# Kernel optimization log

Hardware: AMD Instinct MI355X
Metric: run time of the kernel (lower is better)

Reference implementation:

```python
import jax, jax.numpy as jnp
import numpy as np

RX = 2  # matches init rx
RY = 2  # matches init ry


def _bilinear_gather(img, coords):
    """Bilinear sample with zero padding (mirrors grid_sample align_corners=True, padding_mode='zeros').
    img: [C,H,W]; coords: [P,2] pixel-space (x,y). Returns [C,P]."""
    C, H, W = img.shape
    x, y = coords[:, 0], coords[:, 1]
    x0, y0 = jnp.floor(x), jnp.floor(y)
    wx, wy = x - x0, y - y0

    def tap(xi, yi, w):
        valid = (xi >= 0) & (xi <= W - 1) & (yi >= 0) & (yi <= H - 1)
        xc = jnp.clip(xi, 0, W - 1).astype(jnp.int32)
        yc = jnp.clip(yi, 0, H - 1).astype(jnp.int32)
        v = img[:, yc, xc]  # [C,P] gather
        return v * (w * valid.astype(w.dtype))[None, :]

    return (tap(x0, y0, (1 - wx) * (1 - wy)) + tap(x0 + 1, y0, wx * (1 - wy))
            + tap(x0, y0 + 1, (1 - wx) * wy) + tap(x0 + 1, y0 + 1, wx * wy))


def _local_cost_volume(flow, f1, f2, rx, ry):
    """build_sample_cv: windowed bilinear gather of f2 around (grid + flow), dot with f1.
    Returns cv [N,H,W,2ry+1,2rx+1] with window ordered (dy,dx)."""
    N, C, H, W = f1.shape
    dt = f1.dtype
    gy, gx = jnp.meshgrid(jnp.arange(H, dtype=dt), jnp.arange(W, dtype=dt), indexing='ij')
    base = jnp.stack([gx, gy], 0)[None]            # [1,2,H,W] (x,y) like coords_grid
    cen = (base + flow).transpose(0, 2, 3, 1)       # [N,H,W,2]
    dx = jnp.linspace(-rx, rx, 2 * rx + 1).astype(dt)
    dy = jnp.linspace(-ry, ry, 2 * ry + 1).astype(dt)
    mgy, mgx = jnp.meshgrid(dy, dx, indexing='ij')  # [dH,dW]
    off = jnp.stack([mgx, mgy], -1)                 # [dH,dW,2] (x,y)
    dH, dW = 2 * ry + 1, 2 * rx + 1
    coords = cen[:, None, None] + off[None, :, :, None, None, :]  # [N,dH,dW,H,W,2]
    coords = coords.reshape(N, dH * dW * H * W, 2)
    samp = jax.vmap(_bilinear_gather)(f2, coords)   # [N,C,dH*dW*H*W]
    samp = samp.reshape(N, C, dH, dW, H, W)
    # cv[n,h,w,i,j] = sum_c f1[n,c,h,w] * f2_sampled[n,c,i,j,h,w]
    cv = jnp.einsum('nchw,ncijhw->nhwij', f1, samp)
    return cv


def setup_inputs() -> dict:
    key = jax.random.key(0)
    k1, k2, k3 = jax.random.split(key, 3)
    N, C, H, W = 2, 256, 55, 128
    return {
        'flow': jax.random.normal(k1, (N, 2, H, W), dtype=jnp.float32),
        'f1': jax.random.normal(k2, (N, C, H, W), dtype=jnp.float32),
        'f2': jax.random.normal(k3, (N, C, H, W), dtype=jnp.float32),
    }


def reference(flow, f1, f2):
    cv = _local_cost_volume(flow, f1, f2, RX, RY)   # [N,H,W,dH,dW]
    N, H, W, dH, dW = cv.shape
    flat = cv.reshape(N, H, W, dH * dW)
    # WTA over the last two (window) dims, as in get_argmax_NHW_xy_last_th
    wta_val = jnp.max(flat, axis=-1)
    idx = jnp.argmax(flat, axis=-1)
    wta_xy = jnp.stack([idx % dW, idx // dW], axis=0)  # [2,N,H,W] (x,y)
    return cv, wta_val, wta_xy
```

## Files before the change

kernel.cpp:

```cpp
#include <hip/hip_runtime.h>

#define N_   2
#define C_   256
#define H_   55
#define W_   128
#define HW_  (H_ * W_)
#define NPIX (N_ * HW_)

#define OFF_CV  0
#define OFF_VAL (NPIX * 25)
#define OFF_XY  (OFF_VAL + NPIX)

__global__ __launch_bounds__(256) void transpose_kernel(const float* __restrict__ f1,
                                                        const float* __restrict__ f2,
                                                        float* __restrict__ f1t,
                                                        float* __restrict__ f2t) {
    __shared__ float tile[64][65];
    const int z = blockIdx.z;
    const int n = z & 1;
    const float* __restrict__ src = (z & 2) ? f2 : f1;
    float* __restrict__ dst = (z & 2) ? f2t : f1t;
    src += (size_t)n * C_ * HW_;
    dst += (size_t)n * C_ * HW_;

    const int p0 = blockIdx.x * 64;
    const int c0 = blockIdx.y * 64;
    const int q = threadIdx.x & 15;
    const int r = threadIdx.x >> 4;

    #pragma unroll
    for (int rr = r; rr < 64; rr += 16) {
        const float4 v = *(const float4*)(src + (size_t)(c0 + rr) * HW_ + p0 + q * 4);
        tile[rr][q * 4 + 0] = v.x;
        tile[rr][q * 4 + 1] = v.y;
        tile[rr][q * 4 + 2] = v.z;
        tile[rr][q * 4 + 3] = v.w;
    }
    __syncthreads();

    #pragma unroll
    for (int j = 0; j < 4; ++j) {
        const int pr = r + 16 * j;
        float4 v;
        v.x = tile[q * 4 + 0][pr];
        v.y = tile[q * 4 + 1][pr];
        v.z = tile[q * 4 + 2][pr];
        v.w = tile[q * 4 + 3][pr];
        *(float4*)(dst + (size_t)(p0 + pr) * C_ + c0 + q * 4) = v;
    }
}

__device__ __forceinline__ float dot4(const float4 a, const float4 b) {
    return a.x * b.x + a.y * b.y + a.z * b.z + a.w * b.w;
}

__global__ __launch_bounds__(256) void costvol_kernel(const float* __restrict__ flow,
                                                      const float* __restrict__ f1t,
                                                      const float* __restrict__ f2t,
                                                      float* __restrict__ out) {
    __shared__ float Dsh[4][36];

    const int wv   = threadIdx.x >> 6;
    const int lane = threadIdx.x & 63;
    const int sgrp = lane >> 4;
    const int cgrp = lane & 15;
    const int pix  = blockIdx.x * 4 + wv;
    const int n    = pix / HW_;
    const int rem  = pix - n * HW_;
    const int h    = rem >> 7;
    const int w    = rem & (W_ - 1);

    const float4* __restrict__ arow = (const float4*)(f1t + (size_t)pix * C_) + cgrp * 4;
    const float4 a0 = arow[0], a1 = arow[1], a2 = arow[2], a3 = arow[3];

    const float fx = flow[((size_t)(n * 2 + 0) * H_ + h) * W_ + w];
    const float fy = flow[((size_t)(n * 2 + 1) * H_ + h) * W_ + w];
    const float cx = (float)w + fx;
    const float cy = (float)h + fy;
    const float x0f = floorf(cx), y0f = floorf(cy);
    const float wx = cx - x0f,   wy = cy - y0f;
    const int ix0 = (int)x0f,    iy0 = (int)y0f;

    const float4* __restrict__ f2base =
        (const float4*)(f2t + (size_t)n * HW_ * C_);

    #pragma unroll
    for (int p = 0; p < 9; ++p) {
        const int s  = p * 4 + sgrp;
        const int ly = s / 6, lx = s - ly * 6;
        const int sy = iy0 - 2 + ly;
        const int sx = ix0 - 2 + lx;
        float part = 0.f;
        if (sy >= 0 && sy < H_ && sx >= 0 && sx < W_) {
            const float4* __restrict__ b =
                f2base + (size_t)(sy * W_ + sx) * (C_ / 4) + cgrp * 4;
            part = dot4(a0, b[0]) + dot4(a1, b[1]) + dot4(a2, b[2]) + dot4(a3, b[3]);
        }
        part += __shfl_xor(part, 1, 64);
        part += __shfl_xor(part, 2, 64);
        part += __shfl_xor(part, 4, 64);
        part += __shfl_xor(part, 8, 64);
        if (cgrp == 0) Dsh[wv][s] = part;
    }
    __syncthreads();

    float cv = 0.f;
    if (lane < 25) {
        const int i = lane / 5, j = lane - i * 5;
        const float D00 = Dsh[wv][i * 6 + j];
        const float D01 = Dsh[wv][i * 6 + j + 1];
        const float D10 = Dsh[wv][i * 6 + j + 6];
        const float D11 = Dsh[wv][i * 6 + j + 7];
        cv = (1.f - wx) * (1.f - wy) * D00 + wx * (1.f - wy) * D01
           + (1.f - wx) * wy * D10 + wx * wy * D11;
        out[OFF_CV + (size_t)pix * 25 + lane] = cv;
    }

    float v  = (lane < 25) ? cv : -3.4e38f;
    int  idx = (lane < 25) ? lane : 25;
    #pragma unroll
    for (int off = 16; off >= 1; off >>= 1) {
        const float v2 = __shfl_down(v, off, 32);
        const int   i2 = __shfl_down(idx, off, 32);
        if (v2 > v || (v2 == v && i2 < idx)) { v = v2; idx = i2; }
    }
    if (lane == 0) {
        out[OFF_VAL + pix] = v;
        out[OFF_XY + pix]        = (float)(idx % 5);
        out[OFF_XY + NPIX + pix] = (float)(idx / 5);
    }
}

extern "C" void kernel_launch(void* const* d_in, const int* in_sizes, int n_in,
                              void* d_out, int out_size, void* d_ws, size_t ws_size,
                              hipStream_t stream) {
    const float* flow = (const float*)d_in[0];
    const float* f1   = (const float*)d_in[1];
    const float* f2   = (const float*)d_in[2];
    float* out = (float*)d_out;

    float* f1t = (float*)d_ws;
    float* f2t = f1t + (size_t)N_ * HW_ * C_;

    transpose_kernel<<<dim3(HW_ / 64, C_ / 64, 4), 256, 0, stream>>>(f1, f2, f1t, f2t);
    costvol_kernel<<<dim3(NPIX / 4), 256, 0, stream>>>(flow, f1t, f2t, out);
}
```

Measured before the change: 115.6 us.

## Drop f1 transpose and stage f1 via shared memory; remap blocks per XCD

The separate transpose of f1 is removed. Each cost-volume block now loads its 4 pixels' 256 channels straight from NCHW f1 with one float4 per thread into shared memory, which halves the transpose kernel's traffic. Blocks are also remapped so that consecutive pixel ranges go to the same XCD, aiming to improve L2 locality for the f2t window gathers. The cost is a block-wide sync, and the f1 reads are strided by HW, with each thread reading a 16-byte chunk from a different channel row.

```diff
diff --git a/kernel.cpp b/kernel.cpp
--- a/kernel.cpp
+++ b/kernel.cpp
@@ -6,22 +6,19 @@
 #define W_   128
 #define HW_  (H_ * W_)
 #define NPIX (N_ * HW_)
+#define NBLK (NPIX / 4)
+#define BPX  (NBLK / 8)
 
 #define OFF_CV  0
 #define OFF_VAL (NPIX * 25)
 #define OFF_XY  (OFF_VAL + NPIX)
 
-__global__ __launch_bounds__(256) void transpose_kernel(const float* __restrict__ f1,
-                                                        const float* __restrict__ f2,
-                                                        float* __restrict__ f1t,
-                                                        float* __restrict__ f2t) {
+__global__ __launch_bounds__(256) void transpose_f2(const float* __restrict__ f2,
+                                                    float* __restrict__ f2t) {
     __shared__ float tile[64][65];
-    const int z = blockIdx.z;
-    const int n = z & 1;
-    const float* __restrict__ src = (z & 2) ? f2 : f1;
-    float* __restrict__ dst = (z & 2) ? f2t : f1t;
-    src += (size_t)n * C_ * HW_;
-    dst += (size_t)n * C_ * HW_;
+    const int n = blockIdx.z;
+    const float* __restrict__ src = f2 + (size_t)n * C_ * HW_;
+    float* __restrict__ dst = f2t + (size_t)n * HW_ * C_;
 
     const int p0 = blockIdx.x * 64;
     const int c0 = blockIdx.y * 64;
@@ -55,23 +52,36 @@
 }
 
 __global__ __launch_bounds__(256) void costvol_kernel(const float* __restrict__ flow,
-                                                      const float* __restrict__ f1t,
+                                                      const float* __restrict__ f1,
                                                       const float* __restrict__ f2t,
                                                       float* __restrict__ out) {
+    __shared__ float f1sh[4][C_];
     __shared__ float Dsh[4][36];
+
+    const int b    = blockIdx.x;
+    const int xcd  = b & 7;
+    const int k    = b >> 3;
+    const int pix0 = (xcd * BPX + k) * 4;
+    const int n     = pix0 / HW_;
+    const int prem0 = pix0 - n * HW_;
+
+    {
+        const int t = threadIdx.x;
+        const float4 v = *(const float4*)(f1 + ((size_t)n * C_ + t) * HW_ + prem0);
+        f1sh[0][t] = v.x;
+        f1sh[1][t] = v.y;
+        f1sh[2][t] = v.z;
+        f1sh[3][t] = v.w;
+    }
 
     const int wv   = threadIdx.x >> 6;
     const int lane = threadIdx.x & 63;
     const int sgrp = lane >> 4;
     const int cgrp = lane & 15;
-    const int pix  = blockIdx.x * 4 + wv;
-    const int n    = pix / HW_;
-    const int rem  = pix - n * HW_;
+    const int pix  = pix0 + wv;
+    const int rem  = prem0 + wv;
     const int h    = rem >> 7;
     const int w    = rem & (W_ - 1);
-
-    const float4* __restrict__ arow = (const float4*)(f1t + (size_t)pix * C_) + cgrp * 4;
-    const float4 a0 = arow[0], a1 = arow[1], a2 = arow[2], a3 = arow[3];
 
     const float fx = flow[((size_t)(n * 2 + 0) * H_ + h) * W_ + w];
     const float fy = flow[((size_t)(n * 2 + 1) * H_ + h) * W_ + w];
@@ -80,6 +90,11 @@
     const float x0f = floorf(cx), y0f = floorf(cy);
     const float wx = cx - x0f,   wy = cy - y0f;
     const int ix0 = (int)x0f,    iy0 = (int)y0f;
+
+    __syncthreads();
+
+    const float4* __restrict__ arow = (const float4*)&f1sh[wv][cgrp * 16];
+    const float4 a0 = arow[0], a1 = arow[1], a2 = arow[2], a3 = arow[3];
 
     const float4* __restrict__ f2base =
         (const float4*)(f2t + (size_t)n * HW_ * C_);
@@ -92,9 +107,10 @@
         const int sx = ix0 - 2 + lx;
         float part = 0.f;
         if (sy >= 0 && sy < H_ && sx >= 0 && sx < W_) {
-            const float4* __restrict__ b =
+            const float4* __restrict__ bptr =
                 f2base + (size_t)(sy * W_ + sx) * (C_ / 4) + cgrp * 4;
-            part = dot4(a0, b[0]) + dot4(a1, b[1]) + dot4(a2, b[2]) + dot4(a3, b[3]);
+            part = dot4(a0, bptr[0]) + dot4(a1, bptr[1])
+                 + dot4(a2, bptr[2]) + dot4(a3, bptr[3]);
         }
         part += __shfl_xor(part, 1, 64);
         part += __shfl_xor(part, 2, 64);
@@ -139,9 +155,8 @@
     const float* f2   = (const float*)d_in[2];
     float* out = (float*)d_out;
 
-    float* f1t = (float*)d_ws;
-    float* f2t = f1t + (size_t)N_ * HW_ * C_;
+    float* f2t = (float*)d_ws;
 
-    transpose_kernel<<<dim3(HW_ / 64, C_ / 64, 4), 256, 0, stream>>>(f1, f2, f1t, f2t);
-    costvol_kernel<<<dim3(NPIX / 4), 256, 0, stream>>>(flow, f1t, f2t, out);
+    transpose_f2<<<dim3(HW_ / 64, C_ / 64, N_), 256, 0, stream>>>(f2, f2t);
+    costvol_kernel<<<dim3(NBLK), 256, 0, stream>>>(flow, f1, f2t, out);
 }
```

Measured after the change: 111.7 us. 1.03x faster.
